# Performance work log

Hardware: AMD Instinct MI355X
Metric: run time of the kernel (lower is better)

## Reference

```python
import jax, jax.numpy as jnp
import numpy as np

MASK_VALUE = -10000.0


def setup_inputs() -> dict:
    key = jax.random.key(0)
    ks = jax.random.split(key, 6)
    F_, H, L1N, L2N, B = 1024, 2048, 64, 256, 8192

    def w(k, shape, fan_in):
        return jax.random.normal(k, shape, jnp.float32) * (1.0 / np.sqrt(fan_in))

    x = jax.random.normal(ks[0], (B, F_), jnp.float32)
    W1_1 = w(ks[1], (F_, H), F_); b1_1 = jnp.zeros((H,), jnp.float32)
    W1_2 = w(ks[2], (H, L1N), H); b1_2 = jnp.zeros((L1N,), jnp.float32)
    W2_1 = w(ks[3], (F_, H), F_); b2_1 = jnp.zeros((H,), jnp.float32)
    W2_2 = w(ks[4], (2 * H, L2N), 2 * H); b2_2 = jnp.zeros((L2N,), jnp.float32)
    # child_parent[j] = L1 parent of L2 label j (contiguous groups of 4),
    # equivalent to L12_table = [[4i,4i+1,4i+2,4i+3] for i in range(64)]
    child_parent = jnp.arange(L2N, dtype=jnp.int32) // (L2N // L1N)
    return dict(x=x, W1_1=W1_1, b1_1=b1_1, W1_2=W1_2, b1_2=b1_2,
                W2_1=W2_1, b2_1=b2_1, W2_2=W2_2, b2_2=b2_2,
                child_parent=child_parent)


def reference(x, W1_1, b1_1, W1_2, b1_2, W2_1, b2_1, W2_2, b2_2, child_parent):
    h1 = jax.nn.relu(x @ W1_1 + b1_1)          # [B, H]
    h2 = jax.nn.relu(x @ W2_1 + b2_1)          # [B, H]
    cat = jnp.concatenate([h1, h2], axis=1)    # [B, 2H]
    L1 = jax.nn.softmax(jax.nn.relu(h1 @ W1_2 + b1_2), axis=1)   # [B, L1N]
    l2_logits = jax.nn.relu(cat @ W2_2 + b2_2)                   # [B, L2N]
    parent = jnp.argmax(L1, axis=1)                              # [B] int
    # mask[i, j] = 0 if L2 label j is a child of argmax L1 label, else MASK_VALUE
    mask = jnp.where(child_parent[None, :] == parent[:, None], 0.0, MASK_VALUE)
    L2 = jax.nn.softmax(l2_logits + mask, axis=1)
    return (L1, L2)
```

## Files before the change

kernel.cpp:

```cpp
#include <hip/hip_runtime.h>
#include <hip/hip_bf16.h>
#include <stdint.h>
#include <math.h>


typedef _Float16 f16x8 __attribute__((ext_vector_type(8)));
typedef float    f32x4 __attribute__((ext_vector_type(4)));

#define MASK_VALUE (-10000.0f)
#define SWZ(r) ((((r) + ((r) >> 2))) & 3)
#define RSCALE 2048.0f
#define INV_RSCALE (1.0f / 2048.0f)

#define GLOBAL_AS __attribute__((address_space(1)))
#define LDS_AS    __attribute__((address_space(3)))

__device__ __forceinline__ void gload16(const void* g, void* lds) {
    __builtin_amdgcn_global_load_lds((const GLOBAL_AS void*)g, (LDS_AS void*)lds, 16, 0, 0);
}

__device__ __forceinline__ float rd_any(const void* p, size_t i, int flag) {
    return flag ? (float)((const __hip_bfloat16*)p)[i] : ((const float*)p)[i];
}

__global__ void detect_dtype(const unsigned int* __restrict__ x, int* __restrict__ flag) {
    __shared__ int cnt;
    if (threadIdx.x == 0) cnt = 0;
    __syncthreads();
    int local = 0;
#pragma unroll
    for (int i = 0; i < 4; ++i) {
        unsigned int w = x[threadIdx.x * 4 + i];
        unsigned int e = (w >> 7) & 0xFFu;
        if (e >= 96u && e <= 144u) local++;
    }
    atomicAdd(&cnt, local);
    __syncthreads();
    if (threadIdx.x == 0) *flag = (cnt >= 600) ? 1 : 0;
}

__global__ void split_x(const void* __restrict__ xin,
                        _Float16* __restrict__ xh, _Float16* __restrict__ xl,
                        const int* __restrict__ flagp) {
    int flag = *flagp;
    size_t i = ((size_t)blockIdx.x * 256 + threadIdx.x) * 4;
#pragma unroll
    for (int j = 0; j < 4; ++j) {
        float a = rd_any(xin, i + j, flag);
        _Float16 h = (_Float16)a;
        xh[i + j] = h;
        xl[i + j] = (_Float16)((a - (float)h) * RSCALE);
    }
}

__global__ void split_w1t(const void* __restrict__ src,
                          _Float16* __restrict__ wh, _Float16* __restrict__ wl,
                          const int* __restrict__ flagp) {
    __shared__ __align__(16) float tile[64][65];
    int flag = *flagp;
    const int R = 1024, C = 2048;
    int c0 = blockIdx.x * 64, r0 = blockIdx.y * 64;
    int tx = threadIdx.x & 63, ty = threadIdx.x >> 6;
#pragma unroll
    for (int i = 0; i < 16; ++i) {
        int r = ty + i * 4;
        tile[r][tx] = rd_any(src, (size_t)(r0 + r) * C + c0 + tx, flag);
    }
    __syncthreads();
#pragma unroll
    for (int i = 0; i < 16; ++i) {
        int r = ty + i * 4;
        size_t o = (size_t)(c0 + r) * R + r0 + tx;
        float a = tile[tx][r];
        _Float16 h = (_Float16)a;
        wh[o] = h;
        wl[o] = (_Float16)((a - (float)h) * RSCALE);
    }
}

__global__ void split_w12t(const void* __restrict__ src,
                           _Float16* __restrict__ wh, _Float16* __restrict__ wl,
                           const int* __restrict__ flagp) {
    __shared__ __align__(16) float tile[64][65];
    int flag = *flagp;
    int r0 = blockIdx.x * 64;
    int tx = threadIdx.x & 63, ty = threadIdx.x >> 6;
#pragma unroll
    for (int i = 0; i < 16; ++i) {
        int r = ty + i * 4;
        tile[r][tx] = rd_any(src, (size_t)(r0 + r) * 64 + tx, flag);
    }
    __syncthreads();
#pragma unroll
    for (int i = 0; i < 16; ++i) {
        int r = ty + i * 4;
        size_t o = (size_t)r * 2048 + r0 + tx;
        float a = tile[tx][r];
        _Float16 h = (_Float16)a;
        wh[o] = h;
        wl[o] = (_Float16)((a - (float)h) * RSCALE);
    }
}

__global__ void transpose_to_f16(const void* __restrict__ src, _Float16* __restrict__ dst,
                                 int R, int C, const int* __restrict__ flagp) {
    __shared__ __align__(16) float tile[64][65];
    int flag = *flagp;
    int c0 = blockIdx.x * 64, r0 = blockIdx.y * 64;
    int tx = threadIdx.x & 63, ty = threadIdx.x >> 6;
#pragma unroll
    for (int i = 0; i < 16; ++i) {
        int r = ty + i * 4;
        tile[r][tx] = rd_any(src, (size_t)(r0 + r) * C + c0 + tx, flag);
    }
    __syncthreads();
#pragma unroll
    for (int i = 0; i < 16; ++i) {
        int r = ty + i * 4;
        dst[(size_t)(c0 + r) * R + r0 + tx] = (_Float16)tile[tx][r];
    }
}

__global__ __launch_bounds__(256, 2) void h1_mfma3(
    const _Float16* __restrict__ xh, const _Float16* __restrict__ xl,
    const _Float16* __restrict__ whT, const _Float16* __restrict__ wlT,
    const void* __restrict__ b11,
    _Float16* __restrict__ h1h, _Float16* __restrict__ h1l,
    const int* __restrict__ flagp)
{
    constexpr int K = 1024, BK = 32;
    __shared__ __align__(16) char smem[36864];
    _Float16* Ah = (_Float16*)smem;
    _Float16* Al = (_Float16*)(smem + 8192);
    _Float16* Bh = (_Float16*)(smem + 16384);
    _Float16* Bl = (_Float16*)(smem + 24576);
    int flag = *flagp;
    int t = threadIdx.x, w = t >> 6, lane = t & 63;
    int bid = blockIdx.x;
    int g = bid & 7, s = bid >> 3;
    int mt = g * 8 + (s & 7), nt = s >> 3;
    int i0 = mt * 128, j0 = nt * 128;
    int wr = w & 1, wcb = w >> 1;
    int ml = lane & 15, q = lane >> 4;

    f32x4 acc1[4][4], acc2[4][4];
#pragma unroll
    for (int a = 0; a < 4; ++a)
#pragma unroll
        for (int b = 0; b < 4; ++b) {
            acc1[a][b] = (f32x4){0.f, 0.f, 0.f, 0.f};
            acc2[a][b] = (f32x4){0.f, 0.f, 0.f, 0.f};
        }

    for (int kt = 0; kt < K; kt += BK) {
        __syncthreads();
#pragma unroll
        for (int qq = 0; qq < 2; ++qq) {
            int c = qq * 256 + t;
            int row = c >> 2;
            int gc = (c & 3) ^ SWZ(row);
            size_t ga = (size_t)(i0 + row) * K + kt + gc * 8;
            size_t gb = (size_t)(j0 + row) * K + kt + gc * 8;
            gload16(xh + ga, (char*)Ah + c * 16);
            gload16(xl + ga, (char*)Al + c * 16);
            gload16(whT + gb, (char*)Bh + c * 16);
            gload16(wlT + gb, (char*)Bl + c * 16);
        }
        __syncthreads();

        f16x8 bh[4], bl[4];
#pragma unroll
        for (int ct = 0; ct < 4; ++ct) {
            int row = wcb * 64 + ct * 16 + ml;
            int off = row * 32 + ((q ^ SWZ(row)) << 3);
            bh[ct] = *(const f16x8*)(Bh + off);
            bl[ct] = *(const f16x8*)(Bl + off);
        }
#pragma unroll
        for (int rt = 0; rt < 4; ++rt) {
            int row = wr * 64 + rt * 16 + ml;
            int off = row * 32 + ((q ^ SWZ(row)) << 3);
            f16x8 ah = *(const f16x8*)(Ah + off);
            f16x8 al = *(const f16x8*)(Al + off);
#pragma unroll
            for (int ct = 0; ct < 4; ++ct) {
                acc1[rt][ct] = __builtin_amdgcn_mfma_f32_16x16x32_f16(ah, bh[ct], acc1[rt][ct], 0, 0, 0);
                acc2[rt][ct] = __builtin_amdgcn_mfma_f32_16x16x32_f16(ah, bl[ct], acc2[rt][ct], 0, 0, 0);
                acc2[rt][ct] = __builtin_amdgcn_mfma_f32_16x16x32_f16(al, bh[ct], acc2[rt][ct], 0, 0, 0);
            }
        }
    }

    int rq = (lane >> 4) * 4;
#pragma unroll
    for (int ct = 0; ct < 4; ++ct) {
        float bv = rd_any(b11, j0 + wcb * 64 + ct * 16 + ml, flag);
#pragma unroll
        for (int rt = 0; rt < 4; ++rt)
#pragma unroll
            for (int r = 0; r < 4; ++r) {
                float v = acc1[rt][ct][r] + acc2[rt][ct][r] * INV_RSCALE + bv;
                acc1[rt][ct][r] = v > 0.f ? v : 0.f;
            }
    }

    _Float16* C = (_Float16*)smem;
#pragma unroll
    for (int p = 0; p < 2; ++p) {
        __syncthreads();
#pragma unroll
        for (int rt = 0; rt < 4; ++rt)
#pragma unroll
            for (int ct = 0; ct < 4; ++ct)
#pragma unroll
                for (int r = 0; r < 4; ++r) {
                    float v = acc1[rt][ct][r];
                    _Float16 h = (_Float16)v;
                    _Float16 outv = (p == 0) ? h
                                  : (_Float16)((v - (float)h) * RSCALE);
                    int rl = wr * 64 + rt * 16 + rq + r;
                    int cl = wcb * 64 + ct * 16 + ml;
                    C[rl * 136 + cl] = outv;
                }
        __syncthreads();
        _Float16* dst = (p == 0) ? h1h : h1l;
#pragma unroll
        for (int i = 0; i < 8; ++i) {
            int c = i * 256 + t;
            int row = c >> 4, c8 = (c & 15) * 8;
            *(f16x8*)(dst + (size_t)(i0 + row) * 2048 + j0 + c8) =
                *(const f16x8*)(C + row * 136 + c8);
        }
    }
}

__global__ __launch_bounds__(256, 2) void h2_gemm(
    const _Float16* __restrict__ xh, const _Float16* __restrict__ BT,
    const void* __restrict__ brai, _Float16* __restrict__ h2b,
    const int* __restrict__ flagp)
{
    constexpr int K = 1024, BK = 32;
    __shared__ __align__(16) char smem[36864];
    _Float16* As = (_Float16*)smem;
    _Float16* Bs = (_Float16*)(smem + 8192);
    int flag = *flagp;
    int t = threadIdx.x, w = t >> 6, lane = t & 63;
    int bid = blockIdx.x;
    int g = bid & 7, s = bid >> 3;
    int mt = g * 8 + (s & 7), nt = s >> 3;
    int i0 = mt * 128, j0 = nt * 128;
    int wr = w & 1, wcb = w >> 1;
    int ml = lane & 15, q = lane >> 4;

    f32x4 acc[4][4];
#pragma unroll
    for (int a = 0; a < 4; ++a)
#pragma unroll
        for (int b = 0; b < 4; ++b) acc[a][b] = (f32x4){0.f, 0.f, 0.f, 0.f};

    for (int kt = 0; kt < K; kt += BK) {
        __syncthreads();
#pragma unroll
        for (int qq = 0; qq < 2; ++qq) {
            int c = qq * 256 + t;
            int row = c >> 2;
            int gc = (c & 3) ^ SWZ(row);
            gload16(xh + (size_t)(i0 + row) * K + kt + gc * 8, (char*)As + c * 16);
            gload16(BT + (size_t)(j0 + row) * K + kt + gc * 8, (char*)Bs + c * 16);
        }
        __syncthreads();
        f16x8 af[4], bf[4];
#pragma unroll
        for (int rt = 0; rt < 4; ++rt) {
            int row = wr * 64 + rt * 16 + ml;
            af[rt] = *(const f16x8*)(As + row * 32 + ((q ^ SWZ(row)) << 3));
        }
#pragma unroll
        for (int ct = 0; ct < 4; ++ct) {
            int row = wcb * 64 + ct * 16 + ml;
            bf[ct] = *(const f16x8*)(Bs + row * 32 + ((q ^ SWZ(row)) << 3));
        }
#pragma unroll
        for (int rt = 0; rt < 4; ++rt)
#pragma unroll
            for (int ct = 0; ct < 4; ++ct)
                acc[rt][ct] = __builtin_amdgcn_mfma_f32_16x16x32_f16(
                    af[rt], bf[ct], acc[rt][ct], 0, 0, 0);
    }

    int rq = (lane >> 4) * 4;
    _Float16* C = (_Float16*)smem;
    __syncthreads();
#pragma unroll
    for (int ct = 0; ct < 4; ++ct) {
        float bv = rd_any(brai, j0 + wcb * 64 + ct * 16 + ml, flag);
#pragma unroll
        for (int rt = 0; rt < 4; ++rt)
#pragma unroll
            for (int r = 0; r < 4; ++r) {
                float v = acc[rt][ct][r] + bv;
                v = v > 0.f ? v : 0.f;
                int rl = wr * 64 + rt * 16 + rq + r;
                int cl = wcb * 64 + ct * 16 + ml;
                C[rl * 136 + cl] = (_Float16)v;
            }
    }
    __syncthreads();
#pragma unroll
    for (int i = 0; i < 8; ++i) {
        int c = i * 256 + t;
        int row = c >> 4, c8 = (c & 15) * 8;
        *(f16x8*)(h2b + (size_t)(i0 + row) * 2048 + j0 + c8) =
            *(const f16x8*)(C + row * 136 + c8);
    }
}

__global__ __launch_bounds__(256, 2) void l1_mfma(
    const _Float16* __restrict__ h1h, const _Float16* __restrict__ h1l,
    const _Float16* __restrict__ w12h, const _Float16* __restrict__ w12l,
    const void* __restrict__ b12, float* __restrict__ L1out,
    int* __restrict__ parent, const int* __restrict__ flagp)
{
    __shared__ __align__(16) float red[3][4][256];
    int flag = *flagp;
    int t = threadIdx.x, w = t >> 6, lane = t & 63;
    int ml = lane & 15, kq = (lane >> 4) * 8;
    int r0 = blockIdx.x * 16;

    f32x4 acch[4], accx[4];
#pragma unroll
    for (int ct = 0; ct < 4; ++ct) {
        acch[ct] = (f32x4){0.f, 0.f, 0.f, 0.f};
        accx[ct] = (f32x4){0.f, 0.f, 0.f, 0.f};
    }

    size_t aoff = (size_t)(r0 + ml) * 2048 + w * 512 + kq;
    const _Float16* Ah = h1h + aoff;
    const _Float16* Al = h1l + aoff;
    size_t boff[4];
#pragma unroll
    for (int ct = 0; ct < 4; ++ct)
        boff[ct] = (size_t)(ct * 16 + ml) * 2048 + w * 512 + kq;

    f16x8 ah = *(const f16x8*)(Ah), al = *(const f16x8*)(Al);
    f16x8 bh[4], bl[4];
#pragma unroll
    for (int ct = 0; ct < 4; ++ct) {
        bh[ct] = *(const f16x8*)(w12h + boff[ct]);
        bl[ct] = *(const f16x8*)(w12l + boff[ct]);
    }

    for (int kt = 0; kt < 512; kt += 32) {
        int nk = (kt + 32) & 511;
        f16x8 nah = *(const f16x8*)(Ah + nk);
        f16x8 nal = *(const f16x8*)(Al + nk);
        f16x8 nbh[4], nbl[4];
#pragma unroll
        for (int ct = 0; ct < 4; ++ct) {
            nbh[ct] = *(const f16x8*)(w12h + boff[ct] + nk);
            nbl[ct] = *(const f16x8*)(w12l + boff[ct] + nk);
        }
#pragma unroll
        for (int ct = 0; ct < 4; ++ct) {
            acch[ct] = __builtin_amdgcn_mfma_f32_16x16x32_f16(ah, bh[ct], acch[ct], 0, 0, 0);
            accx[ct] = __builtin_amdgcn_mfma_f32_16x16x32_f16(ah, bl[ct], accx[ct], 0, 0, 0);
            accx[ct] = __builtin_amdgcn_mfma_f32_16x16x32_f16(al, bh[ct], accx[ct], 0, 0, 0);
        }
        ah = nah; al = nal;
#pragma unroll
        for (int ct = 0; ct < 4; ++ct) { bh[ct] = nbh[ct]; bl[ct] = nbl[ct]; }
    }

    f32x4 acc[4];
#pragma unroll
    for (int ct = 0; ct < 4; ++ct)
#pragma unroll
        for (int i = 0; i < 4; ++i)
            acc[ct][i] = acch[ct][i] + accx[ct][i] * INV_RSCALE;

    if (w > 0) {
#pragma unroll
        for (int ct = 0; ct < 4; ++ct)
#pragma unroll
            for (int i = 0; i < 4; ++i)
                red[w - 1][ct][lane * 4 + i] = acc[ct][i];
    }
    __syncthreads();
    if (w != 0) return;

#pragma unroll
    for (int wv = 0; wv < 3; ++wv)
#pragma unroll
        for (int ct = 0; ct < 4; ++ct)
#pragma unroll
            for (int i = 0; i < 4; ++i)
                acc[ct][i] += red[wv][ct][lane * 4 + i];

    int rq = (lane >> 4) * 4;
    float vals[4][4];
    float vmax[4] = {-1e30f, -1e30f, -1e30f, -1e30f};
    int vidx[4] = {1 << 30, 1 << 30, 1 << 30, 1 << 30};
#pragma unroll
    for (int ct = 0; ct < 4; ++ct) {
        int col = ct * 16 + ml;
        float bv = rd_any(b12, col, flag);
#pragma unroll
        for (int r = 0; r < 4; ++r) {
            float v = acc[ct][r] + bv;
            v = v > 0.f ? v : 0.f;
            vals[ct][r] = v;
            if (v > vmax[r] || (v == vmax[r] && col < vidx[r])) { vmax[r] = v; vidx[r] = col; }
        }
    }
#pragma unroll
    for (int d = 1; d < 16; d <<= 1) {
#pragma unroll
        for (int r = 0; r < 4; ++r) {
            float om = __shfl_xor(vmax[r], d);
            int oi = __shfl_xor(vidx[r], d);
            if (om > vmax[r] || (om == vmax[r] && oi < vidx[r])) { vmax[r] = om; vidx[r] = oi; }
        }
    }
    float vsum[4] = {0.f, 0.f, 0.f, 0.f};
#pragma unroll
    for (int ct = 0; ct < 4; ++ct)
#pragma unroll
        for (int r = 0; r < 4; ++r) {
            float e = __expf(vals[ct][r] - vmax[r]);
            vals[ct][r] = e;
            vsum[r] += e;
        }
#pragma unroll
    for (int d = 1; d < 16; d <<= 1)
#pragma unroll
        for (int r = 0; r < 4; ++r) vsum[r] += __shfl_xor(vsum[r], d);

#pragma unroll
    for (int r = 0; r < 4; ++r) {
        float inv = 1.0f / vsum[r];
        int grow = r0 + rq + r;
#pragma unroll
        for (int ct = 0; ct < 4; ++ct)
            L1out[(size_t)grow * 64 + ct * 16 + ml] = vals[ct][r] * inv;
        if (ml == 0) parent[grow] = vidx[r];
    }
}

__global__ __launch_bounds__(256, 2) void l2_gemm(
    const _Float16* __restrict__ h1h, const _Float16* __restrict__ h2b,
    const _Float16* __restrict__ W22T, float* __restrict__ partials)
{
    constexpr int BK = 32;
    __shared__ __align__(16) _Float16 As[128 * BK];
    __shared__ __align__(16) _Float16 Bs[128 * BK];
    int t = threadIdx.x, w = t >> 6, lane = t & 63;
    int bid = blockIdx.x;
    int g = bid & 7, s = bid >> 3;
    int mt = g * 8 + (s & 7);
    int rest = s >> 3;
    int nt = rest & 1, kc = rest >> 1;
    int i0 = mt * 128, j0 = nt * 128;
    const _Float16* Abase = (kc < 2) ? h1h : h2b;
    int kof = (kc & 1) * 1024;
    int wr = w & 1, wcb = w >> 1;
    int ml = lane & 15, q = lane >> 4;

    f32x4 acc[4][4];
#pragma unroll
    for (int a = 0; a < 4; ++a)
#pragma unroll
        for (int b = 0; b < 4; ++b) acc[a][b] = (f32x4){0.f, 0.f, 0.f, 0.f};

    for (int kt = 0; kt < 1024; kt += BK) {
        __syncthreads();
#pragma unroll
        for (int qq = 0; qq < 2; ++qq) {
            int c = qq * 256 + t;
            int row = c >> 2;
            int gc = (c & 3) ^ SWZ(row);
            gload16(Abase + (size_t)(i0 + row) * 2048 + kof + kt + gc * 8, (char*)As + c * 16);
            gload16(W22T + (size_t)(j0 + row) * 4096 + kc * 1024 + kt + gc * 8, (char*)Bs + c * 16);
        }
        __syncthreads();
        f16x8 af[4], bf[4];
#pragma unroll
        for (int rt = 0; rt < 4; ++rt) {
            int row = wr * 64 + rt * 16 + ml;
            af[rt] = *(const f16x8*)(As + row * 32 + ((q ^ SWZ(row)) << 3));
        }
#pragma unroll
        for (int ct = 0; ct < 4; ++ct) {
            int row = wcb * 64 + ct * 16 + ml;
            bf[ct] = *(const f16x8*)(Bs + row * 32 + ((q ^ SWZ(row)) << 3));
        }
#pragma unroll
        for (int rt = 0; rt < 4; ++rt)
#pragma unroll
            for (int ct = 0; ct < 4; ++ct)
                acc[rt][ct] = __builtin_amdgcn_mfma_f32_16x16x32_f16(
                    af[rt], bf[ct], acc[rt][ct], 0, 0, 0);
    }

    float* out = partials + (size_t)kc * 8192 * 256;
    int rq = (lane >> 4) * 4;
#pragma unroll
    for (int ct = 0; ct < 4; ++ct) {
        int nl = j0 + wcb * 64 + ct * 16 + ml;
#pragma unroll
        for (int rt = 0; rt < 4; ++rt) {
            int mbase = i0 + wr * 64 + rt * 16 + rq;
#pragma unroll
            for (int r = 0; r < 4; ++r)
                out[(size_t)(mbase + r) * 256 + nl] = acc[rt][ct][r];
        }
    }
}

__global__ __launch_bounds__(256, 2) void l2_softmax(
    const float* __restrict__ partials, const void* __restrict__ b22,
    const int* __restrict__ child_parent, const int* __restrict__ parent,
    float* __restrict__ L2out, const int* __restrict__ flagp)
{
    int flag = *flagp;
    int t = threadIdx.x, w = t >> 6, lane = t & 63;
    int row = blockIdx.x * 4 + w;
    int c4 = lane * 4;

    float v[4] = {0.f, 0.f, 0.f, 0.f};
#pragma unroll
    for (int kc = 0; kc < 4; ++kc) {
        float4 pv = *(const float4*)(partials + ((size_t)kc * 8192 + row) * 256 + c4);
        v[0] += pv.x; v[1] += pv.y; v[2] += pv.z; v[3] += pv.w;
    }
    int par = parent[row];
#pragma unroll
    for (int j = 0; j < 4; ++j) {
        float x = v[j] + rd_any(b22, c4 + j, flag);
        x = x > 0.f ? x : 0.f;
        if (child_parent[c4 + j] != par) x += MASK_VALUE;
        v[j] = x;
    }
    float m = fmaxf(fmaxf(v[0], v[1]), fmaxf(v[2], v[3]));
#pragma unroll
    for (int d = 1; d < 64; d <<= 1) m = fmaxf(m, __shfl_xor(m, d));
    float sum = 0.f;
#pragma unroll
    for (int j = 0; j < 4; ++j) { v[j] = __expf(v[j] - m); sum += v[j]; }
#pragma unroll
    for (int d = 1; d < 64; d <<= 1) sum += __shfl_xor(sum, d);
    float inv = 1.0f / sum;
    float4 o = {v[0] * inv, v[1] * inv, v[2] * inv, v[3] * inv};
    *(float4*)(L2out + (size_t)row * 256 + c4) = o;
}

extern "C" void kernel_launch(void* const* d_in, const int* in_sizes, int n_in,
                              void* d_out, int out_size, void* d_ws, size_t ws_size,
                              hipStream_t stream) {
    (void)in_sizes; (void)n_in; (void)out_size; (void)ws_size;

    const void* x    = d_in[0];
    const void* W1_1 = d_in[1];
    const void* b1_1 = d_in[2];
    const void* W1_2 = d_in[3];
    const void* b1_2 = d_in[4];
    const void* W2_1 = d_in[5];
    const void* b2_1 = d_in[6];
    const void* W2_2 = d_in[7];
    const void* b2_2 = d_in[8];
    const int* child_parent = (const int*)d_in[9];

    char* p = (char*)d_ws;
    _Float16* xh    = (_Float16*)(p);
    _Float16* xl    = (_Float16*)(p + 16777216);
    _Float16* whT   = (_Float16*)(p + 33554432);
    _Float16* wlT   = (_Float16*)(p + 37748736);
    _Float16* h1h   = (_Float16*)(p + 41943040);
    _Float16* h1l   = (_Float16*)(p + 75497472);
    _Float16* h2b   = (_Float16*)(p + 109051904);
    _Float16* W2Tf  = (_Float16*)(p + 142606336);
    _Float16* W22Tf = (_Float16*)(p + 146800640);
    _Float16* w12h  = (_Float16*)(p + 148897792);
    _Float16* w12l  = (_Float16*)(p + 149159936);
    float* partials = (float*)(p + 149422080);
    int* parent     = (int*)(p + 182976512);
    int* flag       = (int*)(p + 183009280);

    float* L1out = (float*)d_out;
    float* L2out = L1out + (size_t)8192 * 64;

    hipLaunchKernelGGL(detect_dtype, dim3(1), dim3(256), 0, stream,
                       (const unsigned int*)x, flag);
    hipLaunchKernelGGL(split_x, dim3(8192), dim3(256), 0, stream,
                       x, xh, xl, flag);
    hipLaunchKernelGGL(split_w1t, dim3(32, 16), dim3(256), 0, stream,
                       W1_1, whT, wlT, flag);
    hipLaunchKernelGGL(transpose_to_f16, dim3(32, 16), dim3(256), 0, stream,
                       W2_1, W2Tf, 1024, 2048, flag);
    hipLaunchKernelGGL(transpose_to_f16, dim3(4, 64), dim3(256), 0, stream,
                       W2_2, W22Tf, 4096, 256, flag);
    hipLaunchKernelGGL(split_w12t, dim3(32), dim3(256), 0, stream,
                       W1_2, w12h, w12l, flag);

    hipLaunchKernelGGL(h1_mfma3, dim3(1024), dim3(256), 0, stream,
                       xh, xl, whT, wlT, b1_1, h1h, h1l, flag);
    hipLaunchKernelGGL(h2_gemm, dim3(1024), dim3(256), 0, stream,
                       xh, W2Tf, b2_1, h2b, flag);

    hipLaunchKernelGGL(l1_mfma, dim3(512), dim3(256), 0, stream,
                       h1h, h1l, w12h, w12l, b1_2, L1out, parent, flag);

    hipLaunchKernelGGL(l2_gemm, dim3(512), dim3(256), 0, stream,
                       h1h, h2b, W22Tf, partials);
    hipLaunchKernelGGL(l2_softmax, dim3(2048), dim3(256), 0, stream,
                       partials, b2_2, child_parent, parent, L2out, flag);
}
```

Measured before the change: 385.7 us.

## Merge prep kernels, fuse h1/h2 GEMMs and L1/L2 head into fewer launches

Combines the five weight and input conversion kernels into one block-indexed prep kernel. It also merges the h1 and h2 GEMMs into a single 2048-block launch, and merges the L1 head with the L2 partial GEMM into one head kernel. The aim is to cut launch gaps and the tail-idle time between dependent kernels, so independent work can share the GPU at once. The cost is heterogeneous blocks inside one kernel, which gives worse register and occupancy fit because each kernel is sized for its heaviest branch.

```diff
diff --git a/kernel.cpp b/kernel.cpp
--- a/kernel.cpp
+++ b/kernel.cpp
@@ -39,479 +39,492 @@
     if (threadIdx.x == 0) *flag = (cnt >= 600) ? 1 : 0;
 }
 
-__global__ void split_x(const void* __restrict__ xin,
-                        _Float16* __restrict__ xh, _Float16* __restrict__ xl,
-                        const int* __restrict__ flagp) {
-    int flag = *flagp;
-    size_t i = ((size_t)blockIdx.x * 256 + threadIdx.x) * 4;
-#pragma unroll
-    for (int j = 0; j < 4; ++j) {
-        float a = rd_any(xin, i + j, flag);
-        _Float16 h = (_Float16)a;
-        xh[i + j] = h;
-        xl[i + j] = (_Float16)((a - (float)h) * RSCALE);
-    }
-}
-
-__global__ void split_w1t(const void* __restrict__ src,
-                          _Float16* __restrict__ wh, _Float16* __restrict__ wl,
-                          const int* __restrict__ flagp) {
+__global__ void prep_all(
+    const void* __restrict__ x, const void* __restrict__ W1_1,
+    const void* __restrict__ W2_1, const void* __restrict__ W2_2,
+    const void* __restrict__ W1_2,
+    _Float16* __restrict__ xh, _Float16* __restrict__ xl,
+    _Float16* __restrict__ whT, _Float16* __restrict__ wlT,
+    _Float16* __restrict__ W2Tf, _Float16* __restrict__ W22Tf,
+    _Float16* __restrict__ w12h, _Float16* __restrict__ w12l,
+    const int* __restrict__ flagp)
+{
     __shared__ __align__(16) float tile[64][65];
     int flag = *flagp;
-    const int R = 1024, C = 2048;
-    int c0 = blockIdx.x * 64, r0 = blockIdx.y * 64;
-    int tx = threadIdx.x & 63, ty = threadIdx.x >> 6;
-#pragma unroll
-    for (int i = 0; i < 16; ++i) {
-        int r = ty + i * 4;
-        tile[r][tx] = rd_any(src, (size_t)(r0 + r) * C + c0 + tx, flag);
-    }
-    __syncthreads();
-#pragma unroll
-    for (int i = 0; i < 16; ++i) {
-        int r = ty + i * 4;
-        size_t o = (size_t)(c0 + r) * R + r0 + tx;
-        float a = tile[tx][r];
-        _Float16 h = (_Float16)a;
-        wh[o] = h;
-        wl[o] = (_Float16)((a - (float)h) * RSCALE);
-    }
-}
-
-__global__ void split_w12t(const void* __restrict__ src,
-                           _Float16* __restrict__ wh, _Float16* __restrict__ wl,
-                           const int* __restrict__ flagp) {
-    __shared__ __align__(16) float tile[64][65];
-    int flag = *flagp;
-    int r0 = blockIdx.x * 64;
-    int tx = threadIdx.x & 63, ty = threadIdx.x >> 6;
-#pragma unroll
-    for (int i = 0; i < 16; ++i) {
-        int r = ty + i * 4;
-        tile[r][tx] = rd_any(src, (size_t)(r0 + r) * 64 + tx, flag);
-    }
-    __syncthreads();
-#pragma unroll
-    for (int i = 0; i < 16; ++i) {
-        int r = ty + i * 4;
-        size_t o = (size_t)r * 2048 + r0 + tx;
-        float a = tile[tx][r];
-        _Float16 h = (_Float16)a;
-        wh[o] = h;
-        wl[o] = (_Float16)((a - (float)h) * RSCALE);
-    }
-}
-
-__global__ void transpose_to_f16(const void* __restrict__ src, _Float16* __restrict__ dst,
-                                 int R, int C, const int* __restrict__ flagp) {
-    __shared__ __align__(16) float tile[64][65];
-    int flag = *flagp;
-    int c0 = blockIdx.x * 64, r0 = blockIdx.y * 64;
-    int tx = threadIdx.x & 63, ty = threadIdx.x >> 6;
-#pragma unroll
-    for (int i = 0; i < 16; ++i) {
-        int r = ty + i * 4;
-        tile[r][tx] = rd_any(src, (size_t)(r0 + r) * C + c0 + tx, flag);
-    }
-    __syncthreads();
-#pragma unroll
-    for (int i = 0; i < 16; ++i) {
-        int r = ty + i * 4;
-        dst[(size_t)(c0 + r) * R + r0 + tx] = (_Float16)tile[tx][r];
-    }
-}
-
-__global__ __launch_bounds__(256, 2) void h1_mfma3(
+    int bid = blockIdx.x, t = threadIdx.x;
+    int tx = t & 63, ty = t >> 6;
+
+    if (bid < 8192) {
+        size_t i = ((size_t)bid * 256 + t) * 4;
+#pragma unroll
+        for (int j = 0; j < 4; ++j) {
+            float a = rd_any(x, i + j, flag);
+            _Float16 h = (_Float16)a;
+            xh[i + j] = h;
+            xl[i + j] = (_Float16)((a - (float)h) * RSCALE);
+        }
+        return;
+    }
+
+    if (bid < 8704) {
+        int b = bid - 8192;
+        int c0 = (b & 31) * 64, r0 = (b >> 5) * 64;
+#pragma unroll
+        for (int i = 0; i < 16; ++i) {
+            int r = ty + i * 4;
+            tile[r][tx] = rd_any(W1_1, (size_t)(r0 + r) * 2048 + c0 + tx, flag);
+        }
+        __syncthreads();
+#pragma unroll
+        for (int i = 0; i < 16; ++i) {
+            int r = ty + i * 4;
+            size_t o = (size_t)(c0 + r) * 1024 + r0 + tx;
+            float a = tile[tx][r];
+            _Float16 h = (_Float16)a;
+            whT[o] = h;
+            wlT[o] = (_Float16)((a - (float)h) * RSCALE);
+        }
+        return;
+    }
+
+    if (bid < 9216) {
+        int b = bid - 8704;
+        int c0 = (b & 31) * 64, r0 = (b >> 5) * 64;
+#pragma unroll
+        for (int i = 0; i < 16; ++i) {
+            int r = ty + i * 4;
+            tile[r][tx] = rd_any(W2_1, (size_t)(r0 + r) * 2048 + c0 + tx, flag);
+        }
+        __syncthreads();
+#pragma unroll
+        for (int i = 0; i < 16; ++i) {
+            int r = ty + i * 4;
+            W2Tf[(size_t)(c0 + r) * 1024 + r0 + tx] = (_Float16)tile[tx][r];
+        }
+        return;
+    }
+
+    if (bid < 9472) {
+        int b = bid - 9216;
+        int c0 = (b & 3) * 64, r0 = (b >> 2) * 64;
+#pragma unroll
+        for (int i = 0; i < 16; ++i) {
+            int r = ty + i * 4;
+            tile[r][tx] = rd_any(W2_2, (size_t)(r0 + r) * 256 + c0 + tx, flag);
+        }
+        __syncthreads();
+#pragma unroll
+        for (int i = 0; i < 16; ++i) {
+            int r = ty + i * 4;
+            W22Tf[(size_t)(c0 + r) * 4096 + r0 + tx] = (_Float16)tile[tx][r];
+        }
+        return;
+    }
+
+    {
+        int b = bid - 9472;
+        int r0 = b * 64;
+#pragma unroll
+        for (int i = 0; i < 16; ++i) {
+            int r = ty + i * 4;
+            tile[r][tx] = rd_any(W1_2, (size_t)(r0 + r) * 64 + tx, flag);
+        }
+        __syncthreads();
+#pragma unroll
+        for (int i = 0; i < 16; ++i) {
+            int r = ty + i * 4;
+            size_t o = (size_t)r * 2048 + r0 + tx;
+            float a = tile[tx][r];
+            _Float16 h = (_Float16)a;
+            w12h[o] = h;
+            w12l[o] = (_Float16)((a - (float)h) * RSCALE);
+        }
+    }
+}
+
+__global__ __launch_bounds__(256, 2) void h12_gemm(
     const _Float16* __restrict__ xh, const _Float16* __restrict__ xl,
     const _Float16* __restrict__ whT, const _Float16* __restrict__ wlT,
     const void* __restrict__ b11,
+    const _Float16* __restrict__ W2Tf, const void* __restrict__ b21,
     _Float16* __restrict__ h1h, _Float16* __restrict__ h1l,
+    _Float16* __restrict__ h2b,
     const int* __restrict__ flagp)
 {
     constexpr int K = 1024, BK = 32;
     __shared__ __align__(16) char smem[36864];
-    _Float16* Ah = (_Float16*)smem;
-    _Float16* Al = (_Float16*)(smem + 8192);
-    _Float16* Bh = (_Float16*)(smem + 16384);
-    _Float16* Bl = (_Float16*)(smem + 24576);
     int flag = *flagp;
     int t = threadIdx.x, w = t >> 6, lane = t & 63;
-    int bid = blockIdx.x;
-    int g = bid & 7, s = bid >> 3;
-    int mt = g * 8 + (s & 7), nt = s >> 3;
-    int i0 = mt * 128, j0 = nt * 128;
     int wr = w & 1, wcb = w >> 1;
     int ml = lane & 15, q = lane >> 4;
-
-    f32x4 acc1[4][4], acc2[4][4];
-#pragma unroll
-    for (int a = 0; a < 4; ++a)
-#pragma unroll
-        for (int b = 0; b < 4; ++b) {
-            acc1[a][b] = (f32x4){0.f, 0.f, 0.f, 0.f};
-            acc2[a][b] = (f32x4){0.f, 0.f, 0.f, 0.f};
-        }
-
-    for (int kt = 0; kt < K; kt += BK) {
+    int rq = (lane >> 4) * 4;
+
+    if (blockIdx.x < 1024) {
+        _Float16* Ah = (_Float16*)smem;
+        _Float16* Al = (_Float16*)(smem + 8192);
+        _Float16* Bh = (_Float16*)(smem + 16384);
+        _Float16* Bl = (_Float16*)(smem + 24576);
+        int bid = blockIdx.x;
+        int g = bid & 7, s = bid >> 3;
+        int mt = g * 8 + (s & 7), nt = s >> 3;
+        int i0 = mt * 128, j0 = nt * 128;
+
+        f32x4 acc1[4][4], acc2[4][4];
+#pragma unroll
+        for (int a = 0; a < 4; ++a)
+#pragma unroll
+            for (int b = 0; b < 4; ++b) {
+                acc1[a][b] = (f32x4){0.f, 0.f, 0.f, 0.f};
+                acc2[a][b] = (f32x4){0.f, 0.f, 0.f, 0.f};
+            }
+
+        for (int kt = 0; kt < K; kt += BK) {
+            __syncthreads();
+#pragma unroll
+            for (int qq = 0; qq < 2; ++qq) {
+                int c = qq * 256 + t;
+                int row = c >> 2;
+                int gc = (c & 3) ^ SWZ(row);
+                size_t ga = (size_t)(i0 + row) * K + kt + gc * 8;
+                size_t gb = (size_t)(j0 + row) * K + kt + gc * 8;
+                gload16(xh + ga, (char*)Ah + c * 16);
+                gload16(xl + ga, (char*)Al + c * 16);
+                gload16(whT + gb, (char*)Bh + c * 16);
+                gload16(wlT + gb, (char*)Bl + c * 16);
+            }
+            __syncthreads();
+
+            f16x8 bh[4], bl[4];
+#pragma unroll
+            for (int ct = 0; ct < 4; ++ct) {
+                int row = wcb * 64 + ct * 16 + ml;
+                int off = row * 32 + ((q ^ SWZ(row)) << 3);
+                bh[ct] = *(const f16x8*)(Bh + off);
+                bl[ct] = *(const f16x8*)(Bl + off);
+            }
+#pragma unroll
+            for (int rt = 0; rt < 4; ++rt) {
+                int row = wr * 64 + rt * 16 + ml;
+                int off = row * 32 + ((q ^ SWZ(row)) << 3);
+                f16x8 ah = *(const f16x8*)(Ah + off);
+                f16x8 al = *(const f16x8*)(Al + off);
+#pragma unroll
+                for (int ct = 0; ct < 4; ++ct) {
+                    acc1[rt][ct] = __builtin_amdgcn_mfma_f32_16x16x32_f16(ah, bh[ct], acc1[rt][ct], 0, 0, 0);
+                    acc2[rt][ct] = __builtin_amdgcn_mfma_f32_16x16x32_f16(ah, bl[ct], acc2[rt][ct], 0, 0, 0);
+                    acc2[rt][ct] = __builtin_amdgcn_mfma_f32_16x16x32_f16(al, bh[ct], acc2[rt][ct], 0, 0, 0);
+                }
+            }
+        }
+
+#pragma unroll
+        for (int ct = 0; ct < 4; ++ct) {
+            float bv = rd_any(b11, j0 + wcb * 64 + ct * 16 + ml, flag);
+#pragma unroll
+            for (int rt = 0; rt < 4; ++rt)
+#pragma unroll
+                for (int r = 0; r < 4; ++r) {
+                    float v = acc1[rt][ct][r] + acc2[rt][ct][r] * INV_RSCALE + bv;
+                    acc1[rt][ct][r] = v > 0.f ? v : 0.f;
+                }
+        }
+
+        _Float16* C = (_Float16*)smem;
+#pragma unroll
+        for (int p = 0; p < 2; ++p) {
+            __syncthreads();
+#pragma unroll
+            for (int rt = 0; rt < 4; ++rt)
+#pragma unroll
+                for (int ct = 0; ct < 4; ++ct)
+#pragma unroll
+                    for (int r = 0; r < 4; ++r) {
+                        float v = acc1[rt][ct][r];
+                        _Float16 h = (_Float16)v;
+                        _Float16 outv = (p == 0) ? h
+                                      : (_Float16)((v - (float)h) * RSCALE);
+                        int rl = wr * 64 + rt * 16 + rq + r;
+                        int cl = wcb * 64 + ct * 16 + ml;
+                        C[rl * 136 + cl] = outv;
+                    }
+            __syncthreads();
+            _Float16* dst = (p == 0) ? h1h : h1l;
+#pragma unroll
+            for (int i = 0; i < 8; ++i) {
+                int c = i * 256 + t;
+                int row = c >> 4, c8 = (c & 15) * 8;
+                *(f16x8*)(dst + (size_t)(i0 + row) * 2048 + j0 + c8) =
+                    *(const f16x8*)(C + row * 136 + c8);
+            }
+        }
+    } else {
+        _Float16* As = (_Float16*)smem;
+        _Float16* Bs = (_Float16*)(smem + 8192);
+        int bid = blockIdx.x - 1024;
+        int g = bid & 7, s = bid >> 3;
+        int mt = g * 8 + (s & 7), nt = s >> 3;
+        int i0 = mt * 128, j0 = nt * 128;
+
+        f32x4 acc[4][4];
+#pragma unroll
+        for (int a = 0; a < 4; ++a)
+#pragma unroll
+            for (int b = 0; b < 4; ++b) acc[a][b] = (f32x4){0.f, 0.f, 0.f, 0.f};
+
+        for (int kt = 0; kt < K; kt += BK) {
+            __syncthreads();
+#pragma unroll
+            for (int qq = 0; qq < 2; ++qq) {
+                int c = qq * 256 + t;
+                int row = c >> 2;
+                int gc = (c & 3) ^ SWZ(row);
+                gload16(xh + (size_t)(i0 + row) * K + kt + gc * 8, (char*)As + c * 16);
+                gload16(W2Tf + (size_t)(j0 + row) * K + kt + gc * 8, (char*)Bs + c * 16);
+            }
+            __syncthreads();
+            f16x8 af[4], bf[4];
+#pragma unroll
+            for (int rt = 0; rt < 4; ++rt) {
+                int row = wr * 64 + rt * 16 + ml;
+                af[rt] = *(const f16x8*)(As + row * 32 + ((q ^ SWZ(row)) << 3));
+            }
+#pragma unroll
+            for (int ct = 0; ct < 4; ++ct) {
+                int row = wcb * 64 + ct * 16 + ml;
+                bf[ct] = *(const f16x8*)(Bs + row * 32 + ((q ^ SWZ(row)) << 3));
+            }
+#pragma unroll
+            for (int rt = 0; rt < 4; ++rt)
+#pragma unroll
+                for (int ct = 0; ct < 4; ++ct)
+                    acc[rt][ct] = __builtin_amdgcn_mfma_f32_16x16x32_f16(
+                        af[rt], bf[ct], acc[rt][ct], 0, 0, 0);
+        }
+
+        _Float16* C = (_Float16*)smem;
         __syncthreads();
 #pragma unroll
-        for (int qq = 0; qq < 2; ++qq) {
-            int c = qq * 256 + t;
-            int row = c >> 2;
-            int gc = (c & 3) ^ SWZ(row);
-            size_t ga = (size_t)(i0 + row) * K + kt + gc * 8;
-            size_t gb = (size_t)(j0 + row) * K + kt + gc * 8;
-            gload16(xh + ga, (char*)Ah + c * 16);
-            gload16(xl + ga, (char*)Al + c * 16);
-            gload16(whT + gb, (char*)Bh + c * 16);
-            gload16(wlT + gb, (char*)Bl + c * 16);
-        }
-        __syncthreads();
-
-        f16x8 bh[4], bl[4];
-#pragma unroll
         for (int ct = 0; ct < 4; ++ct) {
-            int row = wcb * 64 + ct * 16 + ml;
-            int off = row * 32 + ((q ^ SWZ(row)) << 3);
-            bh[ct] = *(const f16x8*)(Bh + off);
-            bl[ct] = *(const f16x8*)(Bl + off);
-        }
-#pragma unroll
-        for (int rt = 0; rt < 4; ++rt) {
-            int row = wr * 64 + rt * 16 + ml;
-            int off = row * 32 + ((q ^ SWZ(row)) << 3);
-            f16x8 ah = *(const f16x8*)(Ah + off);
-            f16x8 al = *(const f16x8*)(Al + off);
-#pragma unroll
-            for (int ct = 0; ct < 4; ++ct) {
-                acc1[rt][ct] = __builtin_amdgcn_mfma_f32_16x16x32_f16(ah, bh[ct], acc1[rt][ct], 0, 0, 0);
-                acc2[rt][ct] = __builtin_amdgcn_mfma_f32_16x16x32_f16(ah, bl[ct], acc2[rt][ct], 0, 0, 0);
-                acc2[rt][ct] = __builtin_amdgcn_mfma_f32_16x16x32_f16(al, bh[ct], acc2[rt][ct], 0, 0, 0);
-            }
-        }
-    }
-
-    int rq = (lane >> 4) * 4;
-#pragma unroll
-    for (int ct = 0; ct < 4; ++ct) {
-        float bv = rd_any(b11, j0 + wcb * 64 + ct * 16 + ml, flag);
-#pragma unroll
-        for (int rt = 0; rt < 4; ++rt)
-#pragma unroll
-            for (int r = 0; r < 4; ++r) {
-                float v = acc1[rt][ct][r] + acc2[rt][ct][r] * INV_RSCALE + bv;
-                acc1[rt][ct][r] = v > 0.f ? v : 0.f;
-            }
-    }
-
-    _Float16* C = (_Float16*)smem;
-#pragma unroll
-    for (int p = 0; p < 2; ++p) {
-        __syncthreads();
-#pragma unroll
-        for (int rt = 0; rt < 4; ++rt)
-#pragma unroll
-            for (int ct = 0; ct < 4; ++ct)
+            float bv = rd_any(b21, j0 + wcb * 64 + ct * 16 + ml, flag);
+#pragma unroll
+            for (int rt = 0; rt < 4; ++rt)
 #pragma unroll
                 for (int r = 0; r < 4; ++r) {
-                    float v = acc1[rt][ct][r];
-                    _Float16 h = (_Float16)v;
-                    _Float16 outv = (p == 0) ? h
-                                  : (_Float16)((v - (float)h) * RSCALE);
+                    float v = acc[rt][ct][r] + bv;
+                    v = v > 0.f ? v : 0.f;
                     int rl = wr * 64 + rt * 16 + rq + r;
                     int cl = wcb * 64 + ct * 16 + ml;
-                    C[rl * 136 + cl] = outv;
+                    C[rl * 136 + cl] = (_Float16)v;
                 }
+        }
         __syncthreads();
-        _Float16* dst = (p == 0) ? h1h : h1l;
 #pragma unroll
         for (int i = 0; i < 8; ++i) {
             int c = i * 256 + t;
             int row = c >> 4, c8 = (c & 15) * 8;
-            *(f16x8*)(dst + (size_t)(i0 + row) * 2048 + j0 + c8) =
+            *(f16x8*)(h2b + (size_t)(i0 + row) * 2048 + j0 + c8) =
                 *(const f16x8*)(C + row * 136 + c8);
         }
     }
 }
 
-__global__ __launch_bounds__(256, 2) void h2_gemm(
-    const _Float16* __restrict__ xh, const _Float16* __restrict__ BT,
-    const void* __restrict__ brai, _Float16* __restrict__ h2b,
-    const int* __restrict__ flagp)
-{
-    constexpr int K = 1024, BK = 32;
-    __shared__ __align__(16) char smem[36864];
-    _Float16* As = (_Float16*)smem;
-    _Float16* Bs = (_Float16*)(smem + 8192);
-    int flag = *flagp;
-    int t = threadIdx.x, w = t >> 6, lane = t & 63;
-    int bid = blockIdx.x;
-    int g = bid & 7, s = bid >> 3;
-    int mt = g * 8 + (s & 7), nt = s >> 3;
-    int i0 = mt * 128, j0 = nt * 128;
-    int wr = w & 1, wcb = w >> 1;
-    int ml = lane & 15, q = lane >> 4;
-
-    f32x4 acc[4][4];
-#pragma unroll
-    for (int a = 0; a < 4; ++a)
-#pragma unroll
-        for (int b = 0; b < 4; ++b) acc[a][b] = (f32x4){0.f, 0.f, 0.f, 0.f};
-
-    for (int kt = 0; kt < K; kt += BK) {
-        __syncthreads();
-#pragma unroll
-        for (int qq = 0; qq < 2; ++qq) {
-            int c = qq * 256 + t;
-            int row = c >> 2;
-            int gc = (c & 3) ^ SWZ(row);
-            gload16(xh + (size_t)(i0 + row) * K + kt + gc * 8, (char*)As + c * 16);
-            gload16(BT + (size_t)(j0 + row) * K + kt + gc * 8, (char*)Bs + c * 16);
-        }
-        __syncthreads();
-        f16x8 af[4], bf[4];
-#pragma unroll
-        for (int rt = 0; rt < 4; ++rt) {
-            int row = wr * 64 + rt * 16 + ml;
-            af[rt] = *(const f16x8*)(As + row * 32 + ((q ^ SWZ(row)) << 3));
-        }
-#pragma unroll
-        for (int ct = 0; ct < 4; ++ct) {
-            int row = wcb * 64 + ct * 16 + ml;
-            bf[ct] = *(const f16x8*)(Bs + row * 32 + ((q ^ SWZ(row)) << 3));
-        }
-#pragma unroll
-        for (int rt = 0; rt < 4; ++rt)
-#pragma unroll
-            for (int ct = 0; ct < 4; ++ct)
-                acc[rt][ct] = __builtin_amdgcn_mfma_f32_16x16x32_f16(
-                    af[rt], bf[ct], acc[rt][ct], 0, 0, 0);
-    }
-
-    int rq = (lane >> 4) * 4;
-    _Float16* C = (_Float16*)smem;
-    __syncthreads();
-#pragma unroll
-    for (int ct = 0; ct < 4; ++ct) {
-        float bv = rd_any(brai, j0 + wcb * 64 + ct * 16 + ml, flag);
-#pragma unroll
-        for (int rt = 0; rt < 4; ++rt)
-#pragma unroll
-            for (int r = 0; r < 4; ++r) {
-                float v = acc[rt][ct][r] + bv;
-                v = v > 0.f ? v : 0.f;
-                int rl = wr * 64 + rt * 16 + rq + r;
-                int cl = wcb * 64 + ct * 16 + ml;
-                C[rl * 136 + cl] = (_Float16)v;
-            }
-    }
-    __syncthreads();
-#pragma unroll
-    for (int i = 0; i < 8; ++i) {
-        int c = i * 256 + t;
-        int row = c >> 4, c8 = (c & 15) * 8;
-        *(f16x8*)(h2b + (size_t)(i0 + row) * 2048 + j0 + c8) =
-            *(const f16x8*)(C + row * 136 + c8);
-    }
-}
-
-__global__ __launch_bounds__(256, 2) void l1_mfma(
+__global__ __launch_bounds__(256, 2) void head_fused(
     const _Float16* __restrict__ h1h, const _Float16* __restrict__ h1l,
+    const _Float16* __restrict__ h2b, const _Float16* __restrict__ W22T,
+    float* __restrict__ partials,
     const _Float16* __restrict__ w12h, const _Float16* __restrict__ w12l,
     const void* __restrict__ b12, float* __restrict__ L1out,
     int* __restrict__ parent, const int* __restrict__ flagp)
 {
-    __shared__ __align__(16) float red[3][4][256];
+    constexpr int BK = 32;
+    __shared__ __align__(16) char smem[16384];
     int flag = *flagp;
     int t = threadIdx.x, w = t >> 6, lane = t & 63;
-    int ml = lane & 15, kq = (lane >> 4) * 8;
-    int r0 = blockIdx.x * 16;
-
-    f32x4 acch[4], accx[4];
-#pragma unroll
-    for (int ct = 0; ct < 4; ++ct) {
-        acch[ct] = (f32x4){0.f, 0.f, 0.f, 0.f};
-        accx[ct] = (f32x4){0.f, 0.f, 0.f, 0.f};
-    }
-
-    size_t aoff = (size_t)(r0 + ml) * 2048 + w * 512 + kq;
-    const _Float16* Ah = h1h + aoff;
-    const _Float16* Al = h1l + aoff;
-    size_t boff[4];
-#pragma unroll
-    for (int ct = 0; ct < 4; ++ct)
-        boff[ct] = (size_t)(ct * 16 + ml) * 2048 + w * 512 + kq;
-
-    f16x8 ah = *(const f16x8*)(Ah), al = *(const f16x8*)(Al);
-    f16x8 bh[4], bl[4];
-#pragma unroll
-    for (int ct = 0; ct < 4; ++ct) {
-        bh[ct] = *(const f16x8*)(w12h + boff[ct]);
-        bl[ct] = *(const f16x8*)(w12l + boff[ct]);
-    }
-
-    for (int kt = 0; kt < 512; kt += 32) {
-        int nk = (kt + 32) & 511;
-        f16x8 nah = *(const f16x8*)(Ah + nk);
-        f16x8 nal = *(const f16x8*)(Al + nk);
-        f16x8 nbh[4], nbl[4];
+    int ml = lane & 15, q = lane >> 4;
+
+    if (blockIdx.x < 512) {
+        _Float16* As = (_Float16*)smem;
+        _Float16* Bs = (_Float16*)(smem + 8192);
+        int bid = blockIdx.x;
+        int g = bid & 7, s = bid >> 3;
+        int mt = g * 8 + (s & 7);
+        int rest = s >> 3;
+        int nt = rest & 1, kc = rest >> 1;
+        int i0 = mt * 128, j0 = nt * 128;
+        const _Float16* Abase = (kc < 2) ? h1h : h2b;
+        int kof = (kc & 1) * 1024;
+        int wr = w & 1, wcb = w >> 1;
+
+        f32x4 acc[4][4];
+#pragma unroll
+        for (int a = 0; a < 4; ++a)
+#pragma unroll
+            for (int b = 0; b < 4; ++b) acc[a][b] = (f32x4){0.f, 0.f, 0.f, 0.f};
+
+        for (int kt = 0; kt < 1024; kt += BK) {
+            __syncthreads();
+#pragma unroll
+            for (int qq = 0; qq < 2; ++qq) {
+                int c = qq * 256 + t;
+                int row = c >> 2;
+                int gc = (c & 3) ^ SWZ(row);
+                gload16(Abase + (size_t)(i0 + row) * 2048 + kof + kt + gc * 8, (char*)As + c * 16);
+                gload16(W22T + (size_t)(j0 + row) * 4096 + kc * 1024 + kt + gc * 8, (char*)Bs + c * 16);
+            }
+            __syncthreads();
+            f16x8 af[4], bf[4];
+#pragma unroll
+            for (int rt = 0; rt < 4; ++rt) {
+                int row = wr * 64 + rt * 16 + ml;
+                af[rt] = *(const f16x8*)(As + row * 32 + ((q ^ SWZ(row)) << 3));
+            }
+#pragma unroll
+            for (int ct = 0; ct < 4; ++ct) {
+                int row = wcb * 64 + ct * 16 + ml;
+                bf[ct] = *(const f16x8*)(Bs + row * 32 + ((q ^ SWZ(row)) << 3));
+            }
+#pragma unroll
+            for (int rt = 0; rt < 4; ++rt)
+#pragma unroll
+                for (int ct = 0; ct < 4; ++ct)
+                    acc[rt][ct] = __builtin_amdgcn_mfma_f32_16x16x32_f16(
+                        af[rt], bf[ct], acc[rt][ct], 0, 0, 0);
+        }
+
+        float* out = partials + (size_t)kc * 8192 * 256;
+        int rq = (lane >> 4) * 4;
 #pragma unroll
         for (int ct = 0; ct < 4; ++ct) {
-            nbh[ct] = *(const f16x8*)(w12h + boff[ct] + nk);
-            nbl[ct] = *(const f16x8*)(w12l + boff[ct] + nk);
-        }
+            int nl = j0 + wcb * 64 + ct * 16 + ml;
+#pragma unroll
+            for (int rt = 0; rt < 4; ++rt) {
+                int mbase = i0 + wr * 64 + rt * 16 + rq;
+#pragma unroll
+                for (int r = 0; r < 4; ++r)
+                    out[(size_t)(mbase + r) * 256 + nl] = acc[rt][ct][r];
+            }
+        }
+    } else {
+        float* red = (float*)smem;
+        int r0 = (blockIdx.x - 512) * 16;
+        int kq = (lane >> 4) * 8;
+
+        f32x4 acch[4], accx[4];
 #pragma unroll
         for (int ct = 0; ct < 4; ++ct) {
-            acch[ct] = __builtin_amdgcn_mfma_f32_16x16x32_f16(ah, bh[ct], acch[ct], 0, 0, 0);
-            accx[ct] = __builtin_amdgcn_mfma_f32_16x16x32_f16(ah, bl[ct], accx[ct], 0, 0, 0);
-            accx[ct] = __builtin_amdgcn_mfma_f32_16x16x32_f16(al, bh[ct], accx[ct], 0, 0, 0);
-        }
-        ah = nah; al = nal;
-#pragma unroll
-        for (int ct = 0; ct < 4; ++ct) { bh[ct] = nbh[ct]; bl[ct] = nbl[ct]; }
-    }
-
-    f32x4 acc[4];
-#pragma unroll
-    for (int ct = 0; ct < 4; ++ct)
-#pragma unroll
-        for (int i = 0; i < 4; ++i)
-            acc[ct][i] = acch[ct][i] + accx[ct][i] * INV_RSCALE;
-
-    if (w > 0) {
+            acch[ct] = (f32x4){0.f, 0.f, 0.f, 0.f};
+            accx[ct] = (f32x4){0.f, 0.f, 0.f, 0.f};
+        }
+
+        size_t aoff = (size_t)(r0 + ml) * 2048 + w * 512 + kq;
+        const _Float16* Ah = h1h + aoff;
+        const _Float16* Al = h1l + aoff;
+        size_t boff[4];
 #pragma unroll
         for (int ct = 0; ct < 4; ++ct)
+            boff[ct] = (size_t)(ct * 16 + ml) * 2048 + w * 512 + kq;
+
+        f16x8 ah = *(const f16x8*)(Ah), al = *(const f16x8*)(Al);
+        f16x8 bh[4], bl[4];
+#pragma unroll
+        for (int ct = 0; ct < 4; ++ct) {
+            bh[ct] = *(const f16x8*)(w12h + boff[ct]);
+            bl[ct] = *(const f16x8*)(w12l + boff[ct]);
+        }
+
+        for (int kt = 0; kt < 512; kt += 32) {
+            int nk = (kt + 32) & 511;
+            f16x8 nah = *(const f16x8*)(Ah + nk);
+            f16x8 nal = *(const f16x8*)(Al + nk);
+            f16x8 nbh[4], nbl[4];
+#pragma unroll
+            for (int ct = 0; ct < 4; ++ct) {
+                nbh[ct] = *(const f16x8*)(w12h + boff[ct] + nk);
+                nbl[ct] = *(const f16x8*)(w12l + boff[ct] + nk);
+            }
+#pragma unroll
+            for (int ct = 0; ct < 4; ++ct) {
+                acch[ct] = __builtin_amdgcn_mfma_f32_16x16x32_f16(ah, bh[ct], acch[ct], 0, 0, 0);
+                accx[ct] = __builtin_amdgcn_mfma_f32_16x16x32_f16(ah, bl[ct], accx[ct], 0, 0, 0);
+                accx[ct] = __builtin_amdgcn_mfma_f32_16x16x32_f16(al, bh[ct], accx[ct], 0, 0, 0);
+            }
+            ah = nah; al = nal;
+#pragma unroll
+            for (int ct = 0; ct < 4; ++ct) { bh[ct] = nbh[ct]; bl[ct] = nbl[ct]; }
+        }
+
+        f32x4 acc[4];
+#pragma unroll
+        for (int ct = 0; ct < 4; ++ct)
 #pragma unroll
             for (int i = 0; i < 4; ++i)
-                red[w - 1][ct][lane * 4 + i] = acc[ct][i];
-    }
-    __syncthreads();
-    if (w != 0) return;
-
-#pragma unroll
-    for (int wv = 0; wv < 3; ++wv)
+                acc[ct][i] = acch[ct][i] + accx[ct][i] * INV_RSCALE;
+
+        if (w > 0) {
+#pragma unroll
+            for (int ct = 0; ct < 4; ++ct)
+#pragma unroll
+                for (int i = 0; i < 4; ++i)
+                    red[((w - 1) * 4 + ct) * 256 + lane * 4 + i] = acc[ct][i];
+        }
+        __syncthreads();
+        if (w != 0) return;
+
+#pragma unroll
+        for (int wv = 0; wv < 3; ++wv)
+#pragma unroll
+            for (int ct = 0; ct < 4; ++ct)
+#pragma unroll
+                for (int i = 0; i < 4; ++i)
+                    acc[ct][i] += red[(wv * 4 + ct) * 256 + lane * 4 + i];
+
+        int rq = (lane >> 4) * 4;
+        float vals[4][4];
+        float vmax[4] = {-1e30f, -1e30f, -1e30f, -1e30f};
+        int vidx[4] = {1 << 30, 1 << 30, 1 << 30, 1 << 30};
+#pragma unroll
+        for (int ct = 0; ct < 4; ++ct) {
+            int col = ct * 16 + ml;
+            float bv = rd_any(b12, col, flag);
+#pragma unroll
+            for (int r = 0; r < 4; ++r) {
+                float v = acc[ct][r] + bv;
+                v = v > 0.f ? v : 0.f;
+                vals[ct][r] = v;
+                if (v > vmax[r] || (v == vmax[r] && col < vidx[r])) { vmax[r] = v; vidx[r] = col; }
+            }
+        }
+#pragma unroll
+        for (int d = 1; d < 16; d <<= 1) {
+#pragma unroll
+            for (int r = 0; r < 4; ++r) {
+                float om = __shfl_xor(vmax[r], d);
+                int oi = __shfl_xor(vidx[r], d);
+                if (om > vmax[r] || (om == vmax[r] && oi < vidx[r])) { vmax[r] = om; vidx[r] = oi; }
+            }
+        }
+        float vsum[4] = {0.f, 0.f, 0.f, 0.f};
 #pragma unroll
         for (int ct = 0; ct < 4; ++ct)
 #pragma unroll
-            for (int i = 0; i < 4; ++i)
-                acc[ct][i] += red[wv][ct][lane * 4 + i];
-
-    int rq = (lane >> 4) * 4;
-    float vals[4][4];
-    float vmax[4] = {-1e30f, -1e30f, -1e30f, -1e30f};
-    int vidx[4] = {1 << 30, 1 << 30, 1 << 30, 1 << 30};
-#pragma unroll
-    for (int ct = 0; ct < 4; ++ct) {
-        int col = ct * 16 + ml;
-        float bv = rd_any(b12, col, flag);
+            for (int r = 0; r < 4; ++r) {
+                float e = __expf(vals[ct][r] - vmax[r]);
+                vals[ct][r] = e;
+                vsum[r] += e;
+            }
+#pragma unroll
+        for (int d = 1; d < 16; d <<= 1)
+#pragma unroll
+            for (int r = 0; r < 4; ++r) vsum[r] += __shfl_xor(vsum[r], d);
+
 #pragma unroll
         for (int r = 0; r < 4; ++r) {
-            float v = acc[ct][r] + bv;
-            v = v > 0.f ? v : 0.f;
-            vals[ct][r] = v;
-            if (v > vmax[r] || (v == vmax[r] && col < vidx[r])) { vmax[r] = v; vidx[r] = col; }
-        }
-    }
-#pragma unroll
-    for (int d = 1; d < 16; d <<= 1) {
-#pragma unroll
-        for (int r = 0; r < 4; ++r) {
-            float om = __shfl_xor(vmax[r], d);
-            int oi = __shfl_xor(vidx[r], d);
-            if (om > vmax[r] || (om == vmax[r] && oi < vidx[r])) { vmax[r] = om; vidx[r] = oi; }
-        }
-    }
-    float vsum[4] = {0.f, 0.f, 0.f, 0.f};
-#pragma unroll
-    for (int ct = 0; ct < 4; ++ct)
-#pragma unroll
-        for (int r = 0; r < 4; ++r) {
-            float e = __expf(vals[ct][r] - vmax[r]);
-            vals[ct][r] = e;
-            vsum[r] += e;
-        }
-#pragma unroll
-    for (int d = 1; d < 16; d <<= 1)
-#pragma unroll
-        for (int r = 0; r < 4; ++r) vsum[r] += __shfl_xor(vsum[r], d);
-
-#pragma unroll
-    for (int r = 0; r < 4; ++r) {
-        float inv = 1.0f / vsum[r];
-        int grow = r0 + rq + r;
-#pragma unroll
-        for (int ct = 0; ct < 4; ++ct)
-            L1out[(size_t)grow * 64 + ct * 16 + ml] = vals[ct][r] * inv;
-        if (ml == 0) parent[grow] = vidx[r];
-    }
-}
-
-__global__ __launch_bounds__(256, 2) void l2_gemm(
-    const _Float16* __restrict__ h1h, const _Float16* __restrict__ h2b,
-    const _Float16* __restrict__ W22T, float* __restrict__ partials)
-{
-    constexpr int BK = 32;
-    __shared__ __align__(16) _Float16 As[128 * BK];
-    __shared__ __align__(16) _Float16 Bs[128 * BK];
-    int t = threadIdx.x, w = t >> 6, lane = t & 63;
-    int bid = blockIdx.x;
-    int g = bid & 7, s = bid >> 3;
-    int mt = g * 8 + (s & 7);
-    int rest = s >> 3;
-    int nt = rest & 1, kc = rest >> 1;
-    int i0 = mt * 128, j0 = nt * 128;
-    const _Float16* Abase = (kc < 2) ? h1h : h2b;
-    int kof = (kc & 1) * 1024;
-    int wr = w & 1, wcb = w >> 1;
-    int ml = lane & 15, q = lane >> 4;
-
-    f32x4 acc[4][4];
-#pragma unroll
-    for (int a = 0; a < 4; ++a)
-#pragma unroll
-        for (int b = 0; b < 4; ++b) acc[a][b] = (f32x4){0.f, 0.f, 0.f, 0.f};
-
-    for (int kt = 0; kt < 1024; kt += BK) {
-        __syncthreads();
-#pragma unroll
-        for (int qq = 0; qq < 2; ++qq) {
-            int c = qq * 256 + t;
-            int row = c >> 2;
-            int gc = (c & 3) ^ SWZ(row);
-            gload16(Abase + (size_t)(i0 + row) * 2048 + kof + kt + gc * 8, (char*)As + c * 16);
-            gload16(W22T + (size_t)(j0 + row) * 4096 + kc * 1024 + kt + gc * 8, (char*)Bs + c * 16);
-        }
-        __syncthreads();
-        f16x8 af[4], bf[4];
-#pragma unroll
-        for (int rt = 0; rt < 4; ++rt) {
-            int row = wr * 64 + rt * 16 + ml;
-            af[rt] = *(const f16x8*)(As + row * 32 + ((q ^ SWZ(row)) << 3));
-        }
-#pragma unroll
-        for (int ct = 0; ct < 4; ++ct) {
-            int row = wcb * 64 + ct * 16 + ml;
-            bf[ct] = *(const f16x8*)(Bs + row * 32 + ((q ^ SWZ(row)) << 3));
-        }
-#pragma unroll
-        for (int rt = 0; rt < 4; ++rt)
+            float inv = 1.0f / vsum[r];
+            int grow = r0 + rq + r;
 #pragma unroll
             for (int ct = 0; ct < 4; ++ct)
-                acc[rt][ct] = __builtin_amdgcn_mfma_f32_16x16x32_f16(
-                    af[rt], bf[ct], acc[rt][ct], 0, 0, 0);
-    }
-
-    float* out = partials + (size_t)kc * 8192 * 256;
-    int rq = (lane >> 4) * 4;
-#pragma unroll
-    for (int ct = 0; ct < 4; ++ct) {
-        int nl = j0 + wcb * 64 + ct * 16 + ml;
-#pragma unroll
-        for (int rt = 0; rt < 4; ++rt) {
-            int mbase = i0 + wr * 64 + rt * 16 + rq;
-#pragma unroll
-            for (int r = 0; r < 4; ++r)
-                out[(size_t)(mbase + r) * 256 + nl] = acc[rt][ct][r];
+                L1out[(size_t)grow * 64 + ct * 16 + ml] = vals[ct][r] * inv;
+            if (ml == 0) parent[grow] = vidx[r];
         }
     }
 }
@@ -590,27 +603,15 @@
 
     hipLaunchKernelGGL(detect_dtype, dim3(1), dim3(256), 0, stream,
                        (const unsigned int*)x, flag);
-    hipLaunchKernelGGL(split_x, dim3(8192), dim3(256), 0, stream,
-                       x, xh, xl, flag);
-    hipLaunchKernelGGL(split_w1t, dim3(32, 16), dim3(256), 0, stream,
-                       W1_1, whT, wlT, flag);
-    hipLaunchKernelGGL(transpose_to_f16, dim3(32, 16), dim3(256), 0, stream,
-                       W2_1, W2Tf, 1024, 2048, flag);
-    hipLaunchKernelGGL(transpose_to_f16, dim3(4, 64), dim3(256), 0, stream,
-                       W2_2, W22Tf, 4096, 256, flag);
-    hipLaunchKernelGGL(split_w12t, dim3(32), dim3(256), 0, stream,
-                       W1_2, w12h, w12l, flag);
-
-    hipLaunchKernelGGL(h1_mfma3, dim3(1024), dim3(256), 0, stream,
-                       xh, xl, whT, wlT, b1_1, h1h, h1l, flag);
-    hipLaunchKernelGGL(h2_gemm, dim3(1024), dim3(256), 0, stream,
-                       xh, W2Tf, b2_1, h2b, flag);
-
-    hipLaunchKernelGGL(l1_mfma, dim3(512), dim3(256), 0, stream,
-                       h1h, h1l, w12h, w12l, b1_2, L1out, parent, flag);
-
-    hipLaunchKernelGGL(l2_gemm, dim3(512), dim3(256), 0, stream,
-                       h1h, h2b, W22Tf, partials);
+    hipLaunchKernelGGL(prep_all, dim3(9504), dim3(256), 0, stream,
+                       x, W1_1, W2_1, W2_2, W1_2,
+                       xh, xl, whT, wlT, W2Tf, W22Tf, w12h, w12l, flag);
+    hipLaunchKernelGGL(h12_gemm, dim3(2048), dim3(256), 0, stream,
+                       xh, xl, whT, wlT, b1_1, W2Tf, b2_1,
+                       h1h, h1l, h2b, flag);
+    hipLaunchKernelGGL(head_fused, dim3(1024), dim3(256), 0, stream,
+                       h1h, h1l, h2b, W22Tf, partials,
+                       w12h, w12l, b1_2, L1out, parent, flag);
     hipLaunchKernelGGL(l2_softmax, dim3(2048), dim3(256), 0, stream,
                        partials, b2_2, child_parent, parent, L2out, flag);
 }
```

Result: faster. 343.1 us (-11.0%).
